# Kernel optimization log

Hardware: AMD Instinct MI355X
Metric: run time of the kernel (lower is better)

The kernel has to match this reference:

```python
import jax, jax.numpy as jnp
import numpy as np
from jax import ops

N, E, B = 50000, 800000, 64      # nodes, edges, graphs in the batch
D_RAW, D_NAMES = 48, 16          # raw node feats + name embedding -> concat = 64
HID, HEADS = 64, 4               # hidden_dim, num_heads


def setup_inputs() -> dict:
    key = jax.random.key(0)
    ks = iter(jax.random.split(key, 48))
    nrm = lambda shape, s=0.05: jax.random.normal(next(ks), shape, jnp.float32) * s
    inp = dict(
        nfeats=nrm((N, D_RAW), 1.0),
        names=nrm((N, D_NAMES), 1.0),
        centrality=jax.random.uniform(next(ks), (N, 1), jnp.float32) + 0.5,
        edge_weight=jax.random.uniform(next(ks), (E,), jnp.float32),
        src=jax.random.randint(next(ks), (E,), 0, N),
        dst=jax.random.randint(next(ks), (E,), 0, N),
        gid=jnp.sort(jax.random.randint(next(ks), (N,), 0, B)),
    )
    for l in (1, 2, 3):  # three GATConv layers (all in_feats == HID)
        inp[f'W{l}'] = nrm((HID, HEADS * HID))
        inp[f'al{l}'] = nrm((HEADS, HID))
        inp[f'ar{l}'] = nrm((HEADS, HID))
        inp[f'b{l}'] = jnp.zeros((HEADS * HID,), jnp.float32)
    for l in (0, 1, 2, 3):  # four GlobalAttentionPooling gate nets
        inp[f'Wg{l}'] = nrm((HID, 1))
        inp[f'bg{l}'] = jnp.zeros((1,), jnp.float32)
    inp['Wih'] = nrm((4 * HID, HID))
    inp['Whh'] = nrm((4 * HID, HID))
    inp['bih'] = jnp.zeros((4 * HID,), jnp.float32)
    inp['bhh'] = jnp.zeros((4 * HID,), jnp.float32)
    inp['Wc'] = nrm((HID, 1))
    inp['bc'] = jnp.zeros((1,), jnp.float32)
    return inp


def _seg_softmax(e, idx, n):
    """Numerically stable softmax of e over segments given by idx."""
    m = ops.segment_max(e, idx, num_segments=n)
    ex = jnp.exp(e - m[idx])
    s = ops.segment_sum(ex, idx, num_segments=n)
    return ex / s[idx]


def _gat(x, W, al, ar, b, src, dst, ew):
    """DGL GATConv with edge_weight: softmax over incoming edges per dst,
    edge_weight multiplied AFTER the softmax (DGL semantics), bias added."""
    n = x.shape[0]
    ft = (x @ W).reshape(n, HEADS, HID)                 # [N,H,D]
    el = jnp.einsum('nhd,hd->nh', ft, al)
    er = jnp.einsum('nhd,hd->nh', ft, ar)
    e = jax.nn.leaky_relu(el[src] + er[dst], 0.2)       # [E,H]
    a = _seg_softmax(e, dst, n) * ew[:, None]           # [E,H]
    rst = ops.segment_sum(a[:, :, None] * ft[src], dst, num_segments=n)
    return rst + b.reshape(1, HEADS, HID)               # [N,H,D]


def _gap(x, Wg, bg, gid):
    """GlobalAttentionPooling: per-graph softmax gate, weighted node sum."""
    gate = _seg_softmax(x @ Wg + bg, gid, B)            # [N,1]
    return ops.segment_sum(gate * x, gid, num_segments=B)  # [B,D]


def _lstm(xs, Wih, Whh, bih, bhh):
    h = jnp.zeros((xs.shape[1], HID), xs.dtype)
    c = h
    def step(carry, x):
        h, c = carry
        g = x @ Wih.T + bih + h @ Whh.T + bhh
        i, f, gg, o = jnp.split(g, 4, axis=-1)          # torch gate order i,f,g,o
        c = jax.nn.sigmoid(f) * c + jax.nn.sigmoid(i) * jnp.tanh(gg)
        h = jax.nn.sigmoid(o) * jnp.tanh(c)
        return (h, c), h
    (h, _), _ = jax.lax.scan(step, (h, c), xs)
    return h                                            # last hidden state [B,D]


def reference(nfeats, names, centrality, edge_weight, src, dst, gid,
              W1, al1, ar1, b1, W2, al2, ar2, b2, W3, al3, ar3, b3,
              Wg0, bg0, Wg1, bg1, Wg2, bg2, Wg3, bg3,
              Wih, Whh, bih, bhh, Wc, bc):
    x = jnp.concatenate((nfeats, names), axis=1) * centrality
    hg0 = _gap(x, Wg0, bg0, gid)
    h = jax.nn.relu(_gat(x, W1, al1, ar1, b1, src, dst, edge_weight)).mean(axis=1)
    hg1 = _gap(h, Wg1, bg1, gid)
    h = jax.nn.relu(_gat(h, W2, al2, ar2, b2, src, dst, edge_weight)).mean(axis=1)
    hg2 = _gap(h, Wg2, bg2, gid)
    h = jax.nn.relu(_gat(h, W3, al3, ar3, b3, src, dst, edge_weight)).mean(axis=1)
    hg3 = _gap(h, Wg3, bg3, gid)
    seq = jnp.stack((hg0, hg1, hg2, hg3), axis=0)       # [4,B,D]
    hT = _lstm(seq, Wih, Whh, bih, bhh)                 # [B,D]
    return jax.nn.sigmoid(hT @ Wc + bc)                 # [B,1]
```

## Files before the change

kernel.cpp:

```cpp
#include <hip/hip_runtime.h>
#include <hip/hip_bf16.h>

#define N_NODES 50000
#define N_EDGES 800000
#define N_GRAPHS 64
#define SCAN_B 196
#define FT_B   3125
#define GAP_B  512

typedef unsigned short u16;
typedef unsigned char u8;
typedef unsigned int u32;
typedef short s16x8 __attribute__((ext_vector_type(8)));
typedef float f32x4 __attribute__((ext_vector_type(4)));
typedef float f32x2 __attribute__((ext_vector_type(2)));

__device__ __forceinline__ float bf2f(u16 u) {
    union { unsigned int i; float f; } v; v.i = ((unsigned int)u) << 16; return v.f;
}
__device__ __forceinline__ u16 f2bf(float f) {
    union { float f; unsigned int i; } v; v.f = f;
    unsigned int i = v.i;
    unsigned int r = i + 0x7fffu + ((i >> 16) & 1u);
    return (u16)(r >> 16);
}
__device__ __forceinline__ float asfloat(unsigned int u) {
    union { unsigned int i; float f; } v; v.i = u; return v.f;
}

__global__ __launch_bounds__(256) void k_init(const float* __restrict__ nf, const float* __restrict__ nm,
                                              const float* __restrict__ cent, const float* __restrict__ Wg,
                                              const float* __restrict__ bg,
                                              u16* __restrict__ x, float* __restrict__ g,
                                              int* __restrict__ deg) {
    int b = blockIdx.x;
    if (b < SCAN_B) {
        int i = b * 256 + threadIdx.x;
        if (i <= N_NODES) deg[i] = 0;
        return;
    }
    b -= SCAN_B;
    int node = b * 4 + (threadIdx.x >> 6);
    int lane = threadIdx.x & 63;
    float v = (lane < 48) ? nf[(size_t)node * 48 + lane] : nm[(size_t)node * 16 + lane - 48];
    float xf = v * cent[node];
    x[(size_t)node * 64 + lane] = f2bf(xf);
    float p = xf * Wg[lane];
#pragma unroll
    for (int mm = 1; mm < 64; mm <<= 1) p += __shfl_xor(p, mm);
    if (lane == 0) g[node] = p + bg[0];
}

__global__ __launch_bounds__(256) void k_hist(const int* __restrict__ dst, int* __restrict__ deg) {
    int e = blockIdx.x * 256 + threadIdx.x;
    if (e < N_EDGES) atomicAdd(&deg[dst[e]], 1);
}

__global__ __launch_bounds__(256) void k_scanA(const int* __restrict__ deg,
                                               int* __restrict__ rowptr, int* __restrict__ bsum) {
    int b = blockIdx.x, t = threadIdx.x;
    int i = b * 256 + t;
    int v = (i < N_NODES) ? deg[i] : 0;
    int orig = v;
    int lane = t & 63, w = t >> 6;
#pragma unroll
    for (int d = 1; d < 64; d <<= 1) {
        int u = __shfl_up(v, d);
        if (lane >= d) v += u;
    }
    __shared__ int wsum[4];
    if (lane == 63) wsum[w] = v;
    __syncthreads();
    int add = 0;
    for (int k = 0; k < w; k++) add += wsum[k];
    v += add;
    if (i < N_NODES) rowptr[i] = v - orig;
    if (t == 255) bsum[b] = v;
}

__global__ __launch_bounds__(256) void k_scanBprep(const int* __restrict__ bsum, int* __restrict__ boff,
                                                   const float* __restrict__ W1, const float* __restrict__ W2,
                                                   const float* __restrict__ W3, u16* __restrict__ Wt) {
    __shared__ float tile[64][65];
    __shared__ int wsum[4];
    if (blockIdx.x == 0) {
        int t = threadIdx.x;
        int v = (t < SCAN_B) ? bsum[t] : 0;
        int orig = v;
        int lane = t & 63, w = t >> 6;
#pragma unroll
        for (int d = 1; d < 64; d <<= 1) {
            int u = __shfl_up(v, d);
            if (lane >= d) v += u;
        }
        if (lane == 63) wsum[w] = v;
        __syncthreads();
        int add = 0;
        for (int k = 0; k < w; k++) add += wsum[k];
        v += add;
        if (t < SCAN_B) boff[t] = v - orig;
        return;
    }
    int bb = blockIdx.x - 1;
    int l = bb >> 2, ti = bb & 3;
    const float* W = (l == 0) ? W1 : (l == 1) ? W2 : W3;
    u16* o = Wt + (size_t)l * 64 * 256;
    int t = threadIdx.x;
    for (int i = t; i < 64 * 64; i += 256) {
        int d = i >> 6, c = i & 63;
        tile[d][c] = W[d * 256 + ti * 64 + c];
    }
    __syncthreads();
    for (int i = t; i < 64 * 64; i += 256) {
        int c = i >> 6, d = i & 63;
        o[(size_t)(ti * 64 + c) * 64 + d] = f2bf(tile[d][c]);
    }
}

__global__ __launch_bounds__(256) void k_scanC(const int* __restrict__ boff,
                                               int* __restrict__ rowptr, int* __restrict__ deg) {
    int b = blockIdx.x, t = threadIdx.x;
    int i = b * 256 + t;
    if (i < N_NODES) {
        int val = rowptr[i] + boff[b];
        int d = deg[i];
        rowptr[i] = val;
        deg[i] = val;
        if (i == N_NODES - 1) rowptr[N_NODES] = val + d;
    }
}

__global__ __launch_bounds__(256) void k_scatter(const int* __restrict__ src, const int* __restrict__ dst,
                                                 const float* __restrict__ ew, int* __restrict__ cursor,
                                                 u32* __restrict__ csr_se) {
    int e = blockIdx.x * 256 + threadIdx.x;
    if (e < N_EDGES) {
        int d = dst[e];
        int pos = atomicAdd(&cursor[d], 1);
        csr_se[pos] = ((u32)f2bf(ew[e]) << 16) | (u32)src[e];
    }
}

__device__ __forceinline__ void gap_part(int pb, const u16* __restrict__ x, const float* __restrict__ g,
                                         const int* __restrict__ gid,
                                         float* __restrict__ pnum, float* __restrict__ pden) {
    int part = pb & 7, b = pb >> 3;
    int t = threadIdx.x, w = t >> 6, lane = t & 63, q = lane >> 4, c = lane & 15;
    int lo = 0, hi = N_NODES;
    while (lo < hi) { int mid = (lo + hi) >> 1; if (gid[mid] < b) lo = mid + 1; else hi = mid; }
    int s = lo;
    lo = 0; hi = N_NODES;
    while (lo < hi) { int mid = (lo + hi) >> 1; if (gid[mid] < b + 1) lo = mid + 1; else hi = mid; }
    int e = lo;
    int len = e - s;
    int ps = s + (int)(((long long)len * part) >> 3);
    int pe = s + (int)(((long long)len * (part + 1)) >> 3);

    float a0 = 0.f, a1 = 0.f, a2 = 0.f, a3 = 0.f, den = 0.f;
    for (int n0 = ps + w * 4; n0 < pe; n0 += 16) {
        int node = n0 + q;
        if (node < pe) {
            float gate = __expf(fminf(g[node], 30.f));
            uint2 raw = *(const uint2*)(x + (size_t)node * 64 + c * 4);
            a0 = fmaf(gate, asfloat(raw.x << 16), a0);
            a1 = fmaf(gate, asfloat(raw.x & 0xffff0000u), a1);
            a2 = fmaf(gate, asfloat(raw.y << 16), a2);
            a3 = fmaf(gate, asfloat(raw.y & 0xffff0000u), a3);
            if (c == 0) den += gate;
        }
    }
#pragma unroll
    for (int mm = 16; mm < 64; mm <<= 1) {
        a0 += __shfl_xor(a0, mm); a1 += __shfl_xor(a1, mm);
        a2 += __shfl_xor(a2, mm); a3 += __shfl_xor(a3, mm);
        den += __shfl_xor(den, mm);
    }
    __shared__ float snum[4][64];
    __shared__ float sden[4];
    if (lane < 16) {
        snum[w][c * 4 + 0] = a0; snum[w][c * 4 + 1] = a1;
        snum[w][c * 4 + 2] = a2; snum[w][c * 4 + 3] = a3;
        if (lane == 0) sden[w] = den;
    }
    __syncthreads();
    if (t < 64) pnum[((size_t)b * 8 + part) * 64 + t] = snum[0][t] + snum[1][t] + snum[2][t] + snum[3][t];
    if (t == 0) pden[b * 8 + part] = sden[0] + sden[1] + sden[2] + sden[3];
}

__global__ __launch_bounds__(256) void k_ftgap(const u16* __restrict__ X, const u16* __restrict__ Wt,
                                               const float* __restrict__ al, const float* __restrict__ ar,
                                               u8* __restrict__ ft, float* __restrict__ el, float* __restrict__ er,
                                               const float* __restrict__ g, const int* __restrict__ gid,
                                               float* __restrict__ pnum, float* __restrict__ pden) {
    if (blockIdx.x >= FT_B) {
        gap_part(blockIdx.x - FT_B, X, g, gid, pnum, pden);
        return;
    }
    int w = threadIdx.x >> 6;
    int lane = threadIdx.x & 63;
    int quad = lane >> 4, c = lane & 15;
    int n0 = blockIdx.x * 16;

    f32x4 acc[4];
#pragma unroll
    for (int t = 0; t < 4; t++) acc[t] = (f32x4){0.f, 0.f, 0.f, 0.f};

#pragma unroll
    for (int kh = 0; kh < 2; kh++) {
        s16x8 a = *(const s16x8*)(X + (size_t)(n0 + c) * 64 + kh * 32 + quad * 8);
#pragma unroll
        for (int t = 0; t < 4; t++) {
            int col = w * 64 + t * 16 + c;
            s16x8 b = *(const s16x8*)(Wt + (size_t)col * 64 + kh * 32 + quad * 8);
            acc[t] = __builtin_amdgcn_mfma_f32_16x16x32_bf16(a, b, acc[t], 0, 0, 0);
        }
    }

    __shared__ u8 sft[16 * 256];
    float alv[4], arv[4];
#pragma unroll
    for (int t = 0; t < 4; t++) {
        alv[t] = al[w * 64 + t * 16 + c];
        arv[t] = ar[w * 64 + t * 16 + c];
    }
    float pel[4] = {0.f, 0.f, 0.f, 0.f}, per[4] = {0.f, 0.f, 0.f, 0.f};
#pragma unroll
    for (int t = 0; t < 4; t++) {
#pragma unroll
        for (int r = 0; r < 4; r++) {
            float v = acc[t][r];
            int nl = quad * 4 + r;
            int d = t * 16 + c;
            int pk = __builtin_amdgcn_cvt_pk_fp8_f32(v, v, 0, false);
            sft[nl * 256 + d * 4 + w] = (u8)(pk & 0xff);
            pel[r] += v * alv[t];
            per[r] += v * arv[t];
        }
    }
#pragma unroll
    for (int r = 0; r < 4; r++) {
#pragma unroll
        for (int mm = 1; mm < 16; mm <<= 1) {
            pel[r] += __shfl_xor(pel[r], mm);
            per[r] += __shfl_xor(per[r], mm);
        }
    }
    if (c == 0) {
#pragma unroll
        for (int r = 0; r < 4; r++) {
            int node = n0 + quad * 4 + r;
            el[node * 4 + w] = pel[r];
            er[node * 4 + w] = per[r];
        }
    }
    __syncthreads();
    const uint4* s4 = (const uint4*)sft;
    uint4* g4 = (uint4*)(ft + (size_t)n0 * 256);
    g4[threadIdx.x] = s4[threadIdx.x];
}

__global__ __launch_bounds__(256) void k_agg(
    const u8* __restrict__ ft, const float4* __restrict__ el4, const float4* __restrict__ er4,
    const int* __restrict__ rowptr, const u32* __restrict__ csr_se,
    const float* __restrict__ bias, const float* __restrict__ Wg, const float* __restrict__ bg,
    u16* __restrict__ hout, float* __restrict__ gout) {
    int wv = threadIdx.x >> 6;
    int node = blockIdx.x * 4 + wv;
    int lane = threadIdx.x & 63;
    int beg = rowptr[node], end = rowptr[node + 1];
    float4 erv = er4[node];

    __shared__ int    s_off[4][64];
    __shared__ float4 s_p[4][64];

    float S0 = 0.f, S1 = 0.f, S2 = 0.f, S3 = 0.f;
    float a0 = 0.f, a1 = 0.f, a2 = 0.f, a3 = 0.f;

    const char* ftl = (const char*)ft + lane * 4;

    for (int base = beg; base < end; base += 64) {
        int cnt = end - base; if (cnt > 64) cnt = 64;
        if (lane < cnt) {
            u32 se = csr_se[base + lane];
            int sidx = (int)(se & 0xffffu);
            float w = bf2f((u16)(se >> 16));
            float4 elv = el4[sidx];
            float t0 = elv.x + erv.x, t1 = elv.y + erv.y, t2 = elv.z + erv.z, t3 = elv.w + erv.w;
            t0 = t0 > 0.f ? t0 : 0.2f * t0;
            t1 = t1 > 0.f ? t1 : 0.2f * t1;
            t2 = t2 > 0.f ? t2 : 0.2f * t2;
            t3 = t3 > 0.f ? t3 : 0.2f * t3;
            float p0 = __expf(fminf(t0, 30.f));
            float p1 = __expf(fminf(t1, 30.f));
            float p2 = __expf(fminf(t2, 30.f));
            float p3 = __expf(fminf(t3, 30.f));
            S0 += p0; S1 += p1; S2 += p2; S3 += p3;
            s_off[wv][lane] = sidx * 256;
            s_p[wv][lane] = make_float4(p0 * w, p1 * w, p2 * w, p3 * w);
        }
        int k = 0;
        for (; k + 4 <= cnt; k += 4) {
            int o0 = s_off[wv][k], o1 = s_off[wv][k + 1], o2 = s_off[wv][k + 2], o3 = s_off[wv][k + 3];
            unsigned r0 = *(const unsigned*)(ftl + o0);
            unsigned r1 = *(const unsigned*)(ftl + o1);
            unsigned r2 = *(const unsigned*)(ftl + o2);
            unsigned r3 = *(const unsigned*)(ftl + o3);
            float4 q0 = s_p[wv][k], q1 = s_p[wv][k + 1], q2 = s_p[wv][k + 2], q3 = s_p[wv][k + 3];
            f32x2 l0 = __builtin_amdgcn_cvt_pk_f32_fp8(r0, false), h0 = __builtin_amdgcn_cvt_pk_f32_fp8(r0, true);
            f32x2 l1 = __builtin_amdgcn_cvt_pk_f32_fp8(r1, false), h1 = __builtin_amdgcn_cvt_pk_f32_fp8(r1, true);
            f32x2 l2 = __builtin_amdgcn_cvt_pk_f32_fp8(r2, false), h2 = __builtin_amdgcn_cvt_pk_f32_fp8(r2, true);
            f32x2 l3 = __builtin_amdgcn_cvt_pk_f32_fp8(r3, false), h3 = __builtin_amdgcn_cvt_pk_f32_fp8(r3, true);
            a0 = fmaf(q0.x, l0.x, a0); a1 = fmaf(q0.y, l0.y, a1);
            a2 = fmaf(q0.z, h0.x, a2); a3 = fmaf(q0.w, h0.y, a3);
            a0 = fmaf(q1.x, l1.x, a0); a1 = fmaf(q1.y, l1.y, a1);
            a2 = fmaf(q1.z, h1.x, a2); a3 = fmaf(q1.w, h1.y, a3);
            a0 = fmaf(q2.x, l2.x, a0); a1 = fmaf(q2.y, l2.y, a1);
            a2 = fmaf(q2.z, h2.x, a2); a3 = fmaf(q2.w, h2.y, a3);
            a0 = fmaf(q3.x, l3.x, a0); a1 = fmaf(q3.y, l3.y, a1);
            a2 = fmaf(q3.z, h3.x, a2); a3 = fmaf(q3.w, h3.y, a3);
        }
        for (; k < cnt; k++) {
            int o0 = s_off[wv][k];
            float4 q0 = s_p[wv][k];
            unsigned r0 = *(const unsigned*)(ftl + o0);
            f32x2 l0 = __builtin_amdgcn_cvt_pk_f32_fp8(r0, false), h0 = __builtin_amdgcn_cvt_pk_f32_fp8(r0, true);
            a0 = fmaf(q0.x, l0.x, a0); a1 = fmaf(q0.y, l0.y, a1);
            a2 = fmaf(q0.z, h0.x, a2); a3 = fmaf(q0.w, h0.y, a3);
        }
    }
#pragma unroll
    for (int mm = 1; mm < 64; mm <<= 1) {
        S0 += __shfl_xor(S0, mm);
        S1 += __shfl_xor(S1, mm);
        S2 += __shfl_xor(S2, mm);
        S3 += __shfl_xor(S3, mm);
    }
    float i0 = S0 > 0.f ? 1.f / S0 : 0.f;
    float i1 = S1 > 0.f ? 1.f / S1 : 0.f;
    float i2 = S2 > 0.f ? 1.f / S2 : 0.f;
    float i3 = S3 > 0.f ? 1.f / S3 : 0.f;
    float r0 = a0 * i0 + bias[lane];
    float r1 = a1 * i1 + bias[64 + lane];
    float r2 = a2 * i2 + bias[128 + lane];
    float r3 = a3 * i3 + bias[192 + lane];
    float o = (fmaxf(r0, 0.f) + fmaxf(r1, 0.f) + fmaxf(r2, 0.f) + fmaxf(r3, 0.f)) * 0.25f;
    hout[(size_t)node * 64 + lane] = f2bf(o);
    float pg = o * Wg[lane];
#pragma unroll
    for (int mm = 1; mm < 64; mm <<= 1) pg += __shfl_xor(pg, mm);
    if (lane == 0) gout[node] = pg + bg[0];
}

__global__ __launch_bounds__(256) void k_gapP(const u16* __restrict__ x, const float* __restrict__ g,
                                              const int* __restrict__ gid,
                                              float* __restrict__ pnum, float* __restrict__ pden) {
    gap_part(blockIdx.x, x, g, gid, pnum, pden);
}

__global__ __launch_bounds__(256) void k_lstm(const float* __restrict__ pnum, const float* __restrict__ pden,
                                              const float* __restrict__ Wih, const float* __restrict__ Whh,
                                              const float* __restrict__ bih, const float* __restrict__ bhh,
                                              const float* __restrict__ Wc, const float* __restrict__ bc,
                                              float* __restrict__ out) {
    int b = blockIdx.x, t = threadIdx.x;
    __shared__ float h[64], c[64], G[256], xv[64], red[64];
    if (t < 64) { h[t] = 0.f; c[t] = 0.f; }
    __syncthreads();
    for (int step = 0; step < 4; step++) {
        if (t < 64) {
            const float* pn = pnum + (((size_t)step * N_GRAPHS + b) * 8) * 64;
            const float* pd = pden + ((size_t)step * N_GRAPHS + b) * 8;
            float num = 0.f, dn = 0.f;
#pragma unroll
            for (int pp = 0; pp < 8; pp++) { num += pn[pp * 64 + t]; dn += pd[pp]; }
            xv[t] = (dn > 0.f) ? num / dn : 0.f;
        }
        __syncthreads();
        float acc = bih[t] + bhh[t];
#pragma unroll 4
        for (int d = 0; d < 64; d++)
            acc += xv[d] * Wih[t * 64 + d] + h[d] * Whh[t * 64 + d];
        G[t] = acc;
        __syncthreads();
        if (t < 64) {
            float ig = 1.f / (1.f + __expf(-G[t]));
            float fg = 1.f / (1.f + __expf(-G[64 + t]));
            float gg = tanhf(G[128 + t]);
            float og = 1.f / (1.f + __expf(-G[192 + t]));
            float cn = fg * c[t] + ig * gg;
            c[t] = cn;
            h[t] = og * tanhf(cn);
        }
        __syncthreads();
    }
    if (t < 64) red[t] = h[t] * Wc[t];
    __syncthreads();
    if (t == 0) {
        float r = 0.f;
        for (int i = 0; i < 64; i++) r += red[i];
        r += bc[0];
        out[b] = 1.f / (1.f + __expf(-r));
    }
}

extern "C" void kernel_launch(void* const* d_in, const int* in_sizes, int n_in,
                              void* d_out, int out_size, void* d_ws, size_t ws_size,
                              hipStream_t stream) {
    const float* nf   = (const float*)d_in[0];
    const float* nm   = (const float*)d_in[1];
    const float* cent = (const float*)d_in[2];
    const float* ew   = (const float*)d_in[3];
    const int* src  = (const int*)d_in[4];
    const int* dst  = (const int*)d_in[5];
    const int* gid  = (const int*)d_in[6];
    const float* W[3]  = {(const float*)d_in[7],  (const float*)d_in[11], (const float*)d_in[15]};
    const float* al[3] = {(const float*)d_in[8],  (const float*)d_in[12], (const float*)d_in[16]};
    const float* ar[3] = {(const float*)d_in[9],  (const float*)d_in[13], (const float*)d_in[17]};
    const float* bb[3] = {(const float*)d_in[10], (const float*)d_in[14], (const float*)d_in[18]};
    const float* Wg[4] = {(const float*)d_in[19], (const float*)d_in[21], (const float*)d_in[23], (const float*)d_in[25]};
    const float* bg[4] = {(const float*)d_in[20], (const float*)d_in[22], (const float*)d_in[24], (const float*)d_in[26]};
    const float* Wih = (const float*)d_in[27];
    const float* Whh = (const float*)d_in[28];
    const float* bih = (const float*)d_in[29];
    const float* bhh = (const float*)d_in[30];
    const float* Wc  = (const float*)d_in[31];
    const float* bc  = (const float*)d_in[32];
    float* out = (float*)d_out;

    char* p = (char*)d_ws;
    size_t off = 0;
    auto A = [&](size_t bytes) -> char* {
        char* r = p + off;
        off += (bytes + 255) & ~(size_t)255;
        return r;
    };
    u8*    ftb     = (u8*)   A((size_t)N_NODES * 256);
    u16*   nodebuf = (u16*)  A((size_t)N_NODES * 64 * 2);
    u32*   csr_se  = (u32*)  A((size_t)N_EDGES * 4);
    float* el      = (float*)A((size_t)N_NODES * 4 * 4);
    float* er      = (float*)A((size_t)N_NODES * 4 * 4);
    float* gbuf    = (float*)A((size_t)N_NODES * 4);
    int*   rowptr  = (int*)  A((size_t)(N_NODES + 1) * 4);
    int*   deg     = (int*)  A((size_t)(N_NODES + 1) * 4);
    float* pnum    = (float*)A((size_t)4 * N_GRAPHS * 8 * 64 * 4);
    float* pden    = (float*)A((size_t)4 * N_GRAPHS * 8 * 4);
    int*   bsum    = (int*)  A((size_t)SCAN_B * 4);
    int*   boff    = (int*)  A((size_t)SCAN_B * 4);
    u16*   Wt      = (u16*)  A((size_t)3 * 64 * 256 * 2);

    k_init<<<SCAN_B + N_NODES / 4, 256, 0, stream>>>(nf, nm, cent, Wg[0], bg[0], nodebuf, gbuf, deg);
    k_hist<<<(N_EDGES + 255) / 256, 256, 0, stream>>>(dst, deg);
    k_scanA<<<SCAN_B, 256, 0, stream>>>(deg, rowptr, bsum);
    k_scanBprep<<<13, 256, 0, stream>>>(bsum, boff, W[0], W[1], W[2], Wt);
    k_scanC<<<SCAN_B, 256, 0, stream>>>(boff, rowptr, deg);
    k_scatter<<<(N_EDGES + 255) / 256, 256, 0, stream>>>(src, dst, ew, deg, csr_se);

    for (int l = 0; l < 3; l++) {
        k_ftgap<<<FT_B + GAP_B, 256, 0, stream>>>(nodebuf, Wt + (size_t)l * 64 * 256, al[l], ar[l],
                                                  ftb, el, er, gbuf, gid,
                                                  pnum + (size_t)l * N_GRAPHS * 8 * 64,
                                                  pden + (size_t)l * N_GRAPHS * 8);
        k_agg<<<N_NODES / 4, 256, 0, stream>>>(ftb, (const float4*)el, (const float4*)er, rowptr,
                                               csr_se, bb[l], Wg[l + 1], bg[l + 1], nodebuf, gbuf);
    }
    k_gapP<<<GAP_B, 256, 0, stream>>>(nodebuf, gbuf, gid,
                                      pnum + (size_t)3 * N_GRAPHS * 8 * 64,
                                      pden + (size_t)3 * N_GRAPHS * 8);
    k_lstm<<<N_GRAPHS, 256, 0, stream>>>(pnum, pden, Wih, Whh, bih, bhh, Wc, bc, out);
}
```

Baseline: 441.9 us.

## Build CSR via two-pass block-local binning instead of global atomics

Replaces the global-atomic degree histogram and scatter with a two-level radix-style binning. Edges are first bucketed by dst>>8 within 1024-edge chunks using shared-memory atomics. Per-bucket blocks then count degrees and scatter into the CSR, again with shared atomics. This removes contended global atomics and the random global scatter, at the cost of extra intermediate buffers and serial per-thread loops over chunk runs in the second pass.

```diff
diff --git a/kernel.cpp b/kernel.cpp
--- a/kernel.cpp
+++ b/kernel.cpp
@@ -7,6 +7,8 @@
 #define SCAN_B 196
 #define FT_B   3125
 #define GAP_B  512
+#define G1     784
+#define EPB    1024
 
 typedef unsigned short u16;
 typedef unsigned char u8;
@@ -31,16 +33,8 @@
 __global__ __launch_bounds__(256) void k_init(const float* __restrict__ nf, const float* __restrict__ nm,
                                               const float* __restrict__ cent, const float* __restrict__ Wg,
                                               const float* __restrict__ bg,
-                                              u16* __restrict__ x, float* __restrict__ g,
-                                              int* __restrict__ deg) {
-    int b = blockIdx.x;
-    if (b < SCAN_B) {
-        int i = b * 256 + threadIdx.x;
-        if (i <= N_NODES) deg[i] = 0;
-        return;
-    }
-    b -= SCAN_B;
-    int node = b * 4 + (threadIdx.x >> 6);
+                                              u16* __restrict__ x, float* __restrict__ g) {
+    int node = blockIdx.x * 4 + (threadIdx.x >> 6);
     int lane = threadIdx.x & 63;
     float v = (lane < 48) ? nf[(size_t)node * 48 + lane] : nm[(size_t)node * 16 + lane - 48];
     float xf = v * cent[node];
@@ -51,34 +45,77 @@
     if (lane == 0) g[node] = p + bg[0];
 }
 
-__global__ __launch_bounds__(256) void k_hist(const int* __restrict__ dst, int* __restrict__ deg) {
-    int e = blockIdx.x * 256 + threadIdx.x;
-    if (e < N_EDGES) atomicAdd(&deg[dst[e]], 1);
-}
-
-__global__ __launch_bounds__(256) void k_scanA(const int* __restrict__ deg,
-                                               int* __restrict__ rowptr, int* __restrict__ bsum) {
-    int b = blockIdx.x, t = threadIdx.x;
-    int i = b * 256 + t;
-    int v = (i < N_NODES) ? deg[i] : 0;
-    int orig = v;
+__global__ __launch_bounds__(256) void k_bin1(const int* __restrict__ src, const int* __restrict__ dst,
+                                              const float* __restrict__ ew,
+                                              u32* __restrict__ bedge, u8* __restrict__ bdlo,
+                                              int* __restrict__ runstart) {
+    int s = blockIdx.x, t = threadIdx.x;
+    int e0 = s * EPB;
+    int n = N_EDGES - e0; if (n > EPB) n = EPB; if (n < 0) n = 0;
+    __shared__ int lcnt[256];
+    __shared__ int lcur[256];
+    __shared__ int wsum[4];
+    lcnt[t] = 0;
+    __syncthreads();
+    for (int i = t; i < n; i += 256) atomicAdd(&lcnt[dst[e0 + i] >> 8], 1);
+    __syncthreads();
+    int v = lcnt[t], orig = v;
     int lane = t & 63, w = t >> 6;
 #pragma unroll
     for (int d = 1; d < 64; d <<= 1) {
         int u = __shfl_up(v, d);
         if (lane >= d) v += u;
     }
-    __shared__ int wsum[4];
     if (lane == 63) wsum[w] = v;
     __syncthreads();
     int add = 0;
     for (int k = 0; k < w; k++) add += wsum[k];
     v += add;
-    if (i < N_NODES) rowptr[i] = v - orig;
+    int excl = v - orig;
+    if (t < SCAN_B) runstart[s * 197 + t] = excl;
+    if (t == 255) runstart[s * 197 + 196] = v;
+    lcur[t] = excl;
+    __syncthreads();
+    for (int i = t; i < n; i += 256) {
+        int d = dst[e0 + i];
+        int pos = atomicAdd(&lcur[d >> 8], 1);
+        bedge[e0 + pos] = ((u32)f2bf(ew[e0 + i]) << 16) | (u32)src[e0 + i];
+        bdlo[e0 + pos] = (u8)(d & 255);
+    }
+}
+
+__global__ __launch_bounds__(256) void k_cntscan(const int* __restrict__ runstart, const u8* __restrict__ bdlo,
+                                                 int* __restrict__ rowptr, int* __restrict__ bsum) {
+    int b = blockIdx.x, t = threadIdx.x;
+    __shared__ int ndeg[256];
+    __shared__ int wsum[4];
+    ndeg[t] = 0;
+    __syncthreads();
+    for (int s = t; s < G1; s += 256) {
+        int rs = runstart[s * 197 + b], re = runstart[s * 197 + b + 1];
+        const u8* p = bdlo + (size_t)s * EPB;
+        for (int i = rs; i < re; i++) atomicAdd(&ndeg[p[i]], 1);
+    }
+    __syncthreads();
+    int v = ndeg[t], orig = v;
+    int lane = t & 63, w = t >> 6;
+#pragma unroll
+    for (int d = 1; d < 64; d <<= 1) {
+        int u = __shfl_up(v, d);
+        if (lane >= d) v += u;
+    }
+    if (lane == 63) wsum[w] = v;
+    __syncthreads();
+    int add = 0;
+    for (int k = 0; k < w; k++) add += wsum[k];
+    v += add;
+    int node = b * 256 + t;
+    if (node < N_NODES) rowptr[node] = v - orig;
     if (t == 255) bsum[b] = v;
 }
 
 __global__ __launch_bounds__(256) void k_scanBprep(const int* __restrict__ bsum, int* __restrict__ boff,
+                                                   int* __restrict__ rowptr,
                                                    const float* __restrict__ W1, const float* __restrict__ W2,
                                                    const float* __restrict__ W3, u16* __restrict__ Wt) {
     __shared__ float tile[64][65];
@@ -99,6 +136,7 @@
         for (int k = 0; k < w; k++) add += wsum[k];
         v += add;
         if (t < SCAN_B) boff[t] = v - orig;
+        if (t == 0) rowptr[N_NODES] = N_EDGES;
         return;
     }
     int bb = blockIdx.x - 1;
@@ -117,27 +155,26 @@
     }
 }
 
-__global__ __launch_bounds__(256) void k_scanC(const int* __restrict__ boff,
-                                               int* __restrict__ rowptr, int* __restrict__ deg) {
+__global__ __launch_bounds__(256) void k_csr2(int* __restrict__ rowptr, const int* __restrict__ boff,
+                                              const int* __restrict__ runstart, const u32* __restrict__ bedge,
+                                              const u8* __restrict__ bdlo, u32* __restrict__ csr_se) {
     int b = blockIdx.x, t = threadIdx.x;
-    int i = b * 256 + t;
-    if (i < N_NODES) {
-        int val = rowptr[i] + boff[b];
-        int d = deg[i];
-        rowptr[i] = val;
-        deg[i] = val;
-        if (i == N_NODES - 1) rowptr[N_NODES] = val + d;
-    }
-}
-
-__global__ __launch_bounds__(256) void k_scatter(const int* __restrict__ src, const int* __restrict__ dst,
-                                                 const float* __restrict__ ew, int* __restrict__ cursor,
-                                                 u32* __restrict__ csr_se) {
-    int e = blockIdx.x * 256 + threadIdx.x;
-    if (e < N_EDGES) {
-        int d = dst[e];
-        int pos = atomicAdd(&cursor[d], 1);
-        csr_se[pos] = ((u32)f2bf(ew[e]) << 16) | (u32)src[e];
+    __shared__ int cur[256];
+    int node = b * 256 + t;
+    if (node < N_NODES) {
+        int val = rowptr[node] + boff[b];
+        rowptr[node] = val;
+        cur[t] = val;
+    } else cur[t] = 0;
+    __syncthreads();
+    for (int s = t; s < G1; s += 256) {
+        int rs = runstart[s * 197 + b], re = runstart[s * 197 + b + 1];
+        const u32* pe = bedge + (size_t)s * EPB;
+        const u8* pd = bdlo + (size_t)s * EPB;
+        for (int i = rs; i < re; i++) {
+            int pos = atomicAdd(&cur[pd[i]], 1);
+            csr_se[pos] = pe[i];
+        }
     }
 }
 
@@ -437,23 +474,24 @@
     u8*    ftb     = (u8*)   A((size_t)N_NODES * 256);
     u16*   nodebuf = (u16*)  A((size_t)N_NODES * 64 * 2);
     u32*   csr_se  = (u32*)  A((size_t)N_EDGES * 4);
+    u32*   bedge   = (u32*)  A((size_t)G1 * EPB * 4);
+    u8*    bdlo    = (u8*)   A((size_t)G1 * EPB);
+    int*   runstart= (int*)  A((size_t)G1 * 197 * 4);
     float* el      = (float*)A((size_t)N_NODES * 4 * 4);
     float* er      = (float*)A((size_t)N_NODES * 4 * 4);
     float* gbuf    = (float*)A((size_t)N_NODES * 4);
     int*   rowptr  = (int*)  A((size_t)(N_NODES + 1) * 4);
-    int*   deg     = (int*)  A((size_t)(N_NODES + 1) * 4);
     float* pnum    = (float*)A((size_t)4 * N_GRAPHS * 8 * 64 * 4);
     float* pden    = (float*)A((size_t)4 * N_GRAPHS * 8 * 4);
     int*   bsum    = (int*)  A((size_t)SCAN_B * 4);
     int*   boff    = (int*)  A((size_t)SCAN_B * 4);
     u16*   Wt      = (u16*)  A((size_t)3 * 64 * 256 * 2);
 
-    k_init<<<SCAN_B + N_NODES / 4, 256, 0, stream>>>(nf, nm, cent, Wg[0], bg[0], nodebuf, gbuf, deg);
-    k_hist<<<(N_EDGES + 255) / 256, 256, 0, stream>>>(dst, deg);
-    k_scanA<<<SCAN_B, 256, 0, stream>>>(deg, rowptr, bsum);
-    k_scanBprep<<<13, 256, 0, stream>>>(bsum, boff, W[0], W[1], W[2], Wt);
-    k_scanC<<<SCAN_B, 256, 0, stream>>>(boff, rowptr, deg);
-    k_scatter<<<(N_EDGES + 255) / 256, 256, 0, stream>>>(src, dst, ew, deg, csr_se);
+    k_init<<<N_NODES / 4, 256, 0, stream>>>(nf, nm, cent, Wg[0], bg[0], nodebuf, gbuf);
+    k_bin1<<<G1, 256, 0, stream>>>(src, dst, ew, bedge, bdlo, runstart);
+    k_cntscan<<<SCAN_B, 256, 0, stream>>>(runstart, bdlo, rowptr, bsum);
+    k_scanBprep<<<13, 256, 0, stream>>>(bsum, boff, rowptr, W[0], W[1], W[2], Wt);
+    k_csr2<<<SCAN_B, 256, 0, stream>>>(rowptr, boff, runstart, bedge, bdlo, csr_se);
 
     for (int l = 0; l < 3; l++) {
         k_ftgap<<<FT_B + GAP_B, 256, 0, stream>>>(nodebuf, Wt + (size_t)l * 64 * 256, al[l], ar[l],
```

Result: faster. 388.5 us, median of 2 (-12.1%).
